# Optimization experiments

Hardware: AMD Instinct MI355X
Metric: run time of the kernel (lower is better)

## Reference

```python
import jax, jax.numpy as jnp
import numpy as np

B, N, T = 32, 256, 256
W, H, EMB = 32, 128, 64          # window_size, tgcn_hidden_dim, gsl_embed_dim
K, ALPHA, NC, E = 3, 1.0, 16, 8192  # gsl_avg_steps, gsl_alpha, num_classes, static edges
GCN_IN = W + H                    # GSL gconv in_channels
THRESH = 1e-8


def setup_inputs():
    ks = jax.random.split(jax.random.key(0), 24)
    rng = np.random.default_rng(0)
    src = rng.integers(0, N, size=E)
    tgt = (src + 1 + rng.integers(0, N - 1, size=E)) % N  # no self-loops (PyG adds them)
    edge_index = jnp.asarray(np.stack([src, tgt]), dtype=jnp.int32)

    def p(k, shape):
        return jax.random.normal(k, shape, jnp.float32) * (shape[0] ** -0.5)

    z = lambda n: jnp.zeros((n,), jnp.float32)
    return {
        "x": jax.random.normal(ks[0], (B, N, T), jnp.float32),
        "static_edge_index": edge_index,
        "static_edge_weight": jax.random.uniform(ks[1], (E,), jnp.float32),
        "Wg": p(ks[2], (GCN_IN, EMB)), "bg": z(EMB),
        "W1": p(ks[3], (EMB, EMB)), "b1": z(EMB),
        "W2": p(ks[4], (EMB, EMB)), "b2": z(EMB),
        "Wz": p(ks[5], (W, H)), "bz": z(H),
        "Wr": p(ks[6], (W, H)), "br": z(H),
        "Wh": p(ks[7], (W, H)), "bh": z(H),
        "Wlz": p(ks[8], (2 * H, H)), "blz": z(H),
        "Wlr": p(ks[9], (2 * H, H)), "blr": z(H),
        "Wlh": p(ks[10], (2 * H, H)), "blh": z(H),
        "Wc": p(ks[11], (H * N, NC)), "bc": z(NC),
    }


def _forward(x, edge_index, edge_weight, Wg, bg, W1, b1, W2, b2,
             Wz, bz, Wr, br, Wh, bh, Wlz, blz, Wlr, blr, Wlh, blh, Wc, bc):
    dt = x.dtype
    eye = jnp.eye(N, dtype=dt)

    # Static graph: dense adjacency + self loops, symmetric GCN normalization.
    A = jnp.zeros((N, N), dt).at[edge_index[0], edge_index[1]].add(edge_weight) + eye
    deg = A.sum(0)  # in-degree at targets (col sums)
    di = jnp.where(deg > 0, jax.lax.rsqrt(deg), 0.0)
    S = di[:, None] * A * di[None, :]  # S[r,c]; out[c] = sum_r S[r,c] x[r]

    # windowing: v[t,b,n,:] = x[b,n,t*W:(t+1)*W]
    v = x.reshape(B, N, T // W, W).transpose(2, 0, 1, 3)  # [nw,B,N,W]

    def gcn_norm_b(Ad):  # Ad [B,N,N], zero diagonal guaranteed
        Ah = Ad + eye
        d = Ah.sum(-2)
        q = jnp.where(d > 0, jax.lax.rsqrt(d), 0.0)
        return q[:, :, None] * Ah * q[:, None, :]

    def step(carry, vt):
        h, hist, cnt = carry  # h [B,N,H], hist [K,B,N,N]
        It = jnp.concatenate([vt, h], -1)                   # [B,N,W+H]
        df = jnp.einsum('rc,brf->bcf', S, It @ Wg) + bg     # static GCNConv
        de1 = jnp.tanh(ALPHA * (df @ W1 + b1))
        de2 = jnp.tanh(ALPHA * (df @ W2 + b2))
        M = jnp.einsum('bne,bme->bnm', de1, de2)            # de1 @ de2^T
        Et = jax.nn.relu(jnp.tanh(ALPHA * (M - M.transpose(0, 2, 1))))
        hist = jnp.concatenate([hist[1:], Et[None]], 0)     # deque(maxlen=K)
        cnt = jnp.minimum(cnt + 1, K)
        Mt = hist.sum(0) / cnt.astype(dt)
        An = gcn_norm_b(jnp.where(Mt > THRESH, Mt, jnp.zeros((), dt)))

        def conv(Wk, bk):  # dynamic GCNConv, block-diag == per-batch dense
            return jnp.einsum('brc,brf->bcf', An, vt @ Wk) + bk

        Z = jax.nn.sigmoid(jnp.concatenate([conv(Wz, bz), h], -1) @ Wlz + blz)
        R = jax.nn.sigmoid(jnp.concatenate([conv(Wr, br), h], -1) @ Wlr + blr)
        Ht = jnp.tanh(jnp.concatenate([conv(Wh, bh), h * R], -1) @ Wlh + blh)
        h = Z * h + (1.0 - Z) * Ht
        return (h, hist, cnt), None

    h0 = jnp.zeros((B, N, H), dt)
    hist0 = jnp.zeros((K, B, N, N), dt)
    (h, _, _), _ = jax.lax.scan(step, (h0, hist0, jnp.int32(0)), v)
    return h.reshape(B, N * H) @ Wc + bc  # [B, NC]


def reference(x, static_edge_index, static_edge_weight, Wg, bg, W1, b1, W2, b2,
              Wz, bz, Wr, br, Wh, bh, Wlz, blz, Wlr, blr, Wlh, blh, Wc, bc):
    return _forward(x, static_edge_index, static_edge_weight, Wg, bg, W1, b1, W2, b2,
                    Wz, bz, Wr, br, Wh, bh, Wlz, blz, Wlr, blr, Wlh, blh, Wc, bc)
```

## Files before the change

### kernel.cpp

```cpp
#include <hip/hip_runtime.h>
#include <hip/hip_bf16.h>
#include <math.h>

#define BB  32
#define NN  256
#define TT  256
#define WW  32
#define HH  128
#define EMBD 64
#define NCLS 16
#define NE  8192

__device__ __forceinline__ float bf(const __hip_bfloat16* p, int i) {
    return __bfloat162float(p[i]);
}
__device__ __forceinline__ float ld3(const void* p, int i, int m) {
    if (m == 2) return (float)((const double*)p)[i];
    if (m == 1) return ((const float*)p)[i];
    return __bfloat162float(((const __hip_bfloat16*)p)[i]);
}
__device__ __forceinline__ float r16(float x) {
    return __bfloat162float(__float2bfloat16(x));
}
__device__ __forceinline__ float tanh_s(float x) {
    x = fminf(20.0f, fmaxf(-20.0f, x));
    return tanhf(x);
}
__device__ __forceinline__ float sig_s(float x) {
    x = fminf(30.0f, fmaxf(-30.0f, x));
    return 1.0f / (1.0f + expf(-x));
}


__global__ __launch_bounds__(64) void k_sentinel(float* out, float v) {
    int i = blockIdx.x * 64 + threadIdx.x;
    if (i < BB * NCLS) out[i] = v;
}

__global__ __launch_bounds__(256) void k_probe_all(
        const void* x, const void* ew, const void* Wg, const void* W1, const void* W2,
        const void* Wz, const void* Wr, const void* Wh, const void* Wlz, const void* Wlr,
        const void* Wlh, const void* Wc, int* insB, int* insF) {
    int sec = blockIdx.x >> 2, sub = blockIdx.x & 3;
    const void* p; int nB, idx;
    switch (sec) {
        case 0:  p = x;   nB = 32768; idx = 0;  break;
        case 1:  p = ew;  nB = 8192;  idx = 2;  break;
        case 2:  p = Wg;  nB = 10240; idx = 3;  break;
        case 3:  p = W1;  nB = 4096;  idx = 5;  break;
        case 4:  p = W2;  nB = 4096;  idx = 7;  break;
        case 5:  p = Wz;  nB = 4096;  idx = 9;  break;
        case 6:  p = Wr;  nB = 4096;  idx = 11; break;
        case 7:  p = Wh;  nB = 4096;  idx = 13; break;
        case 8:  p = Wlz; nB = 32768; idx = 15; break;
        case 9:  p = Wlr; nB = 32768; idx = 17; break;
        case 10: p = Wlh; nB = 32768; idx = 19; break;
        default: p = Wc;  nB = 32768; idx = 21; break;
    }
    int nF = nB >> 2;
    const __hip_bfloat16* pb = (const __hip_bfloat16*)p;
    const float* pf = (const float*)p;
    int start = sub * 256 + threadIdx.x;
    for (int i = start; i < nB; i += 1024) {
        float v = __bfloat162float(pb[i]);
        if (!(fabsf(v) < 64.0f)) { insB[idx] = 1; break; }
    }
    for (int i = start; i < nF; i += 1024) {
        float v = pf[i];
        if (!(fabsf(v) < 1e4f)) { insF[idx] = 1; break; }
    }
}

__global__ void k_resolve(const int* insB, const int* insF, int* modes) {
    int i = threadIdx.x;
    if (i < 32 && i != 1)
        modes[i] = insB[i] ? (insF[i] ? 2 : 1) : 0;
}

__global__ __launch_bounds__(64) void k_detect_ei(const int* ei, int* modes) {
    if (threadIdx.x == 0 && blockIdx.x == 0) {
        bool allz = true;
        for (int k = 1; k < 64; k += 2) if (ei[k] != 0) allz = false;
        modes[1] = allz ? 1 : 0;
    }
}

__global__ __launch_bounds__(256) void k_cvtall(const void* Wg, const void* W1, const void* W2,
                                                const void* Wz, const void* Wr, const void* Wh,
                                                const void* Wlz, const void* Wlr, const void* Wlh,
                                                const void* Wc, const int* modes, float* dst) {
    int i = blockIdx.x * 256 + threadIdx.x;
    if (i >= 665600) return;
    float v;
    if      (i < 10240)  v = ld3(Wg,  i,          modes[3]);
    else if (i < 14336)  v = ld3(W1,  i - 10240,  modes[5]);
    else if (i < 18432)  v = ld3(W2,  i - 14336,  modes[7]);
    else if (i < 22528)  v = ld3(Wz,  i - 18432,  modes[9]);
    else if (i < 26624)  v = ld3(Wr,  i - 22528,  modes[11]);
    else if (i < 30720)  v = ld3(Wh,  i - 26624,  modes[13]);
    else if (i < 63488)  v = ld3(Wlz, i - 30720,  modes[15]);
    else if (i < 96256)  v = ld3(Wlr, i - 63488,  modes[17]);
    else if (i < 129024) v = ld3(Wlh, i - 96256,  modes[19]);
    else if (i < 653312) v = ld3(Wc,  i - 129024, modes[21]);
    else {
        int j = i - 653312, w = j / 384, rem = j - w * 384;
        int g = rem >> 7, f = rem & 127;
        const void* Wk = (g == 0) ? Wz : ((g == 1) ? Wr : Wh);
        int mk = (g == 0) ? modes[9] : ((g == 1) ? modes[11] : modes[13]);
        v = ld3(Wk, w * 128 + f, mk);
    }
    dst[i] = v;
}

__global__ __launch_bounds__(256) void k_fuse(const float* Wzf, const float* Wrf, const float* Whf,
                                              const float* Wlzf, const float* Wlrf, const float* Wlhf,
                                              const __hip_bfloat16* bz, const __hip_bfloat16* br,
                                              const __hip_bfloat16* bh,
                                              const __hip_bfloat16* blz, const __hip_bfloat16* blr,
                                              const __hip_bfloat16* blh,
                                              float* Wf, float* bfv) {
    int g = blockIdx.y;
    const float* Wcv = (g == 0) ? Wzf : ((g == 1) ? Wrf : Whf);
    const float* Wl  = (g == 0) ? Wlzf : ((g == 1) ? Wlrf : Wlhf);
    const __hip_bfloat16* bcv = (g == 0) ? bz : ((g == 1) ? br : bh);
    const __hip_bfloat16* blv = (g == 0) ? blz : ((g == 1) ? blr : blh);
    int idx = blockIdx.x * 256 + threadIdx.x;
    if (idx >= 160 * 128) return;
    int k = idx >> 7, f = idx & 127;
    float v;
    if (k < 32) {
        float acc = 0.f;
        for (int m = 0; m < 128; m++) acc += Wcv[k * 128 + m] * Wl[m * 128 + f];
        v = acc;
    } else {
        v = Wl[(k + 96) * 128 + f];
    }
    Wf[((size_t)g * 160 + k) * 128 + f] = v;
    if (idx < 128) {
        float acc = __bfloat162float(blv[idx]);
        for (int m = 0; m < 128; m++) acc += __bfloat162float(bcv[m]) * Wl[m * 128 + idx];
        bfv[g * 128 + idx] = acc;
    }
}


__global__ __launch_bounds__(256) void k_scatter(const int* ei, const void* ew, float* A,
                                                 const int* modes) {
    int e = blockIdx.x * 256 + threadIdx.x;
    if (e < NE) {
        int s, t;
        if (modes[1]) { s = ei[2 * e]; t = ei[2 * (NE + e)]; }
        else          { s = ei[e];     t = ei[NE + e]; }
        float w = r16(ld3(ew, e, modes[2]));
        if ((unsigned)s < NN && (unsigned)t < NN)
            atomicAdd(&A[s * NN + t], w);
    }
    if (blockIdx.x == 0) atomicAdd(&A[threadIdx.x * NN + threadIdx.x], 1.0f);
}

__global__ __launch_bounds__(256) void k_roundA(float* A) {
    int i = blockIdx.x * 256 + threadIdx.x;
    A[i] = r16(A[i]);
}

__global__ __launch_bounds__(256) void k_di(const float* A, float* di) {
    int wave = threadIdx.x >> 6, lane = threadIdx.x & 63;
    int c = blockIdx.x * 4 + wave;
    float s = 0.f;
    for (int r = lane; r < NN; r += 64) s += A[r * NN + c];
    for (int o = 32; o > 0; o >>= 1) s += __shfl_down(s, o, 64);
    if (lane == 0) {
        float deg = r16(s);
        di[c] = (deg > 0.f) ? r16(1.0f / sqrtf(deg)) : 0.0f;
    }
}

__global__ __launch_bounds__(256) void k_St(const float* A, const float* di, float* St) {
    int idx = blockIdx.x * 256 + threadIdx.x;
    int c = idx >> 8, r = idx & 255;
    St[idx] = r16(r16(di[r] * A[r * NN + c]) * di[c]);
}


__global__ __launch_bounds__(256) void k1_itwg4(const void* x, const float* h,
                                                const float* Wgf, float* Y,
                                                int t, const int* modes) {
    __shared__ float vt[4][32];
    __shared__ float hr[4][128];
    int b = blockIdx.y, n0 = blockIdx.x * 4;
    int tid = threadIdx.x;
    int nd = tid >> 6, f = tid & 63;
    if (f < WW) vt[nd][f] = ld3(x, (b * NN + n0 + nd) * TT + t * WW + f, modes[0]);
    size_t hb = (size_t)(b * NN + n0 + nd) * HH;
    hr[nd][f] = h[hb + f];
    hr[nd][f + 64] = h[hb + f + 64];
    __syncthreads();
    float acc = 0.f;
    for (int k = 0; k < WW; k++)  acc += vt[nd][k] * Wgf[k * EMBD + f];
    for (int k = 0; k < HH; k++)  acc += hr[nd][k] * Wgf[(WW + k) * EMBD + f];
    if (t == 0 && modes[0] == 0 && modes[3] == 0) acc = r16(acc);
    Y[(size_t)(b * NN + n0 + nd) * EMBD + f] = acc;
}

__global__ __launch_bounds__(256) void k23g(const float* St, const float* Y,
                                            const __hip_bfloat16* bg,
                                            const float* W1f, const float* W2f,
                                            const __hip_bfloat16* b1, const __hip_bfloat16* b2,
                                            float* de1, float* de2, float* qsum,
                                            int t, const int* modes) {
    __shared__ float As[32][36];
    __shared__ float Bs[32][68];
    __shared__ float dfT[64][36];
    int b = blockIdx.y, c0 = blockIdx.x * 32;
    int tid = threadIdx.x;
    if (blockIdx.x == 0) qsum[b * NN + tid] = 0.f;
    int tm = tid >> 4, tn = tid & 15;
    int am = tid & 31, ak0 = (tid >> 5) * 4;
    int bk = tid >> 3, bn0 = (tid & 7) * 8;
    const float* Yb = Y + (size_t)b * (NN * EMBD);
    float acc[2][4] = {};
    for (int kb = 0; kb < 256; kb += 32) {
        float4 a0 = *(const float4*)(St + (size_t)(c0 + am) * 256 + kb + ak0);
        float av4[4] = {a0.x, a0.y, a0.z, a0.w};
        int rot = (tid >> 5) & 3;
#pragma unroll
        for (int jj = 0; jj < 4; jj++) { int j = (jj + rot) & 3; As[ak0 + j][am] = av4[j]; }
        const float* bp = Yb + (size_t)(kb + bk) * 64 + bn0;
        *(float4*)&Bs[bk][bn0]     = *(const float4*)bp;
        *(float4*)&Bs[bk][bn0 + 4] = *(const float4*)(bp + 4);
        __syncthreads();
#pragma unroll
        for (int kk = 0; kk < 32; kk++) {
            float2 av = *(const float2*)&As[kk][tm * 2];
            float4 bv = *(const float4*)&Bs[kk][tn * 4];
            float aa[2] = {av.x, av.y};
            float bb[4] = {bv.x, bv.y, bv.z, bv.w};
#pragma unroll
            for (int i = 0; i < 2; i++)
#pragma unroll
                for (int j = 0; j < 4; j++) acc[i][j] += aa[i] * bb[j];
        }
        __syncthreads();
    }
    bool rnd = (t == 0 && modes[0] == 0 && modes[3] == 0);
#pragma unroll
    for (int i = 0; i < 2; i++)
#pragma unroll
        for (int j = 0; j < 4; j++) {
            int f = tn * 4 + j;
            float v = (rnd ? r16(acc[i][j]) : acc[i][j]) + bf(bg, f);
            dfT[f][tm * 2 + i] = v;
        }
    __syncthreads();
    float a1acc[2][4] = {};
    for (int kb2 = 0; kb2 < 64; kb2 += 32) {
        const float* bp = W1f + (size_t)(kb2 + bk) * 64 + bn0;
        *(float4*)&Bs[bk][bn0]     = *(const float4*)bp;
        *(float4*)&Bs[bk][bn0 + 4] = *(const float4*)(bp + 4);
        __syncthreads();
#pragma unroll
        for (int kk = 0; kk < 32; kk++) {
            float2 av = *(const float2*)&dfT[kb2 + kk][tm * 2];
            float4 bv = *(const float4*)&Bs[kk][tn * 4];
            float aa[2] = {av.x, av.y};
            float bb[4] = {bv.x, bv.y, bv.z, bv.w};
#pragma unroll
            for (int i = 0; i < 2; i++)
#pragma unroll
                for (int j = 0; j < 4; j++) a1acc[i][j] += aa[i] * bb[j];
        }
        __syncthreads();
    }
#pragma unroll
    for (int i = 0; i < 2; i++) {
        int row = b * NN + c0 + tm * 2 + i;
        float4 o;
        o.x = tanh_s(a1acc[i][0] + bf(b1, tn * 4 + 0));
        o.y = tanh_s(a1acc[i][1] + bf(b1, tn * 4 + 1));
        o.z = tanh_s(a1acc[i][2] + bf(b1, tn * 4 + 2));
        o.w = tanh_s(a1acc[i][3] + bf(b1, tn * 4 + 3));
        *(float4*)&de1[(size_t)row * 64 + tn * 4] = o;
    }
    float a2acc[2][4] = {};
    for (int kb2 = 0; kb2 < 64; kb2 += 32) {
        const float* bp = W2f + (size_t)(kb2 + bk) * 64 + bn0;
        *(float4*)&Bs[bk][bn0]     = *(const float4*)bp;
        *(float4*)&Bs[bk][bn0 + 4] = *(const float4*)(bp + 4);
        __syncthreads();
#pragma unroll
        for (int kk = 0; kk < 32; kk++) {
            float2 av = *(const float2*)&dfT[kb2 + kk][tm * 2];
            float4 bv = *(const float4*)&Bs[kk][tn * 4];
            float aa[2] = {av.x, av.y};
            float bb[4] = {bv.x, bv.y, bv.z, bv.w};
#pragma unroll
            for (int i = 0; i < 2; i++)
#pragma unroll
                for (int j = 0; j < 4; j++) a2acc[i][j] += aa[i] * bb[j];
        }
        __syncthreads();
    }
#pragma unroll
    for (int i = 0; i < 2; i++) {
        int row = b * NN + c0 + tm * 2 + i;
        float4 o;
        o.x = tanh_s(a2acc[i][0] + bf(b2, tn * 4 + 0));
        o.y = tanh_s(a2acc[i][1] + bf(b2, tn * 4 + 1));
        o.z = tanh_s(a2acc[i][2] + bf(b2, tn * 4 + 2));
        o.w = tanh_s(a2acc[i][3] + bf(b2, tn * 4 + 3));
        *(float4*)&de2[(size_t)row * 64 + tn * 4] = o;
    }
}

__global__ __launch_bounds__(256) void k45(const float* de1, const float* de2,
                                           float* hist, float* AhT, float* qsum,
                                           int slabW, int slabR, float inv_cnt) {
    __shared__ float As[32][68];
    __shared__ float Bs[32][68];
    __shared__ float m2b[64][65];
    __shared__ float qpart[64];
    int b = blockIdx.z, r0 = blockIdx.x * 64, c0 = blockIdx.y * 64;
    int tid = threadIdx.x;
    if (tid < 64) qpart[tid] = 0.f;
    int tn = tid & 15, tm = tid >> 4;
    int am = tid >> 2, ak0 = (tid & 3) * 8;
    int rot = (tid & 3) * 2;
    const float* d1 = de1 + (size_t)b * (NN * EMBD);
    const float* d2 = de2 + (size_t)b * (NN * EMBD);
    float acc2[4][4] = {};
    for (int kb = 0; kb < 64; kb += 32) {
        const float* ap = d1 + (size_t)(c0 + am) * 64 + kb + ak0;
        float4 a0 = *(const float4*)ap;
        float4 a1 = *(const float4*)(ap + 4);
        float av8[8] = {a0.x, a0.y, a0.z, a0.w, a1.x, a1.y, a1.z, a1.w};
#pragma unroll
        for (int jj = 0; jj < 8; jj++) { int j = (jj + rot) & 7; As[ak0 + j][am] = av8[j]; }
        const float* bp = d2 + (size_t)(r0 + am) * 64 + kb + ak0;
        float4 b0 = *(const float4*)bp;
        float4 b1v = *(const float4*)(bp + 4);
        float bv8[8] = {b0.x, b0.y, b0.z, b0.w, b1v.x, b1v.y, b1v.z, b1v.w};
#pragma unroll
        for (int jj = 0; jj < 8; jj++) { int j = (jj + rot) & 7; Bs[ak0 + j][am] = bv8[j]; }
        __syncthreads();
#pragma unroll
        for (int kk = 0; kk < 32; kk++) {
            float4 av = *(const float4*)&As[kk][tm * 4];
            float4 bv = *(const float4*)&Bs[kk][tn * 4];
            float aa[4] = {av.x, av.y, av.z, av.w};
            float bb[4] = {bv.x, bv.y, bv.z, bv.w};
#pragma unroll
            for (int i = 0; i < 4; i++)
#pragma unroll
                for (int j = 0; j < 4; j++) acc2[i][j] += aa[i] * bb[j];
        }
        __syncthreads();
    }
#pragma unroll
    for (int i = 0; i < 4; i++)
#pragma unroll
        for (int j = 0; j < 4; j++) m2b[tm * 4 + i][tn * 4 + j] = acc2[i][j];
    float acc1[4][4] = {};
    for (int kb = 0; kb < 64; kb += 32) {
        const float* ap = d1 + (size_t)(r0 + am) * 64 + kb + ak0;
        float4 a0 = *(const float4*)ap;
        float4 a1 = *(const float4*)(ap + 4);
        float av8[8] = {a0.x, a0.y, a0.z, a0.w, a1.x, a1.y, a1.z, a1.w};
#pragma unroll
        for (int jj = 0; jj < 8; jj++) { int j = (jj + rot) & 7; As[ak0 + j][am] = av8[j]; }
        const float* bp = d2 + (size_t)(c0 + am) * 64 + kb + ak0;
        float4 b0 = *(const float4*)bp;
        float4 b1v = *(const float4*)(bp + 4);
        float bv8[8] = {b0.x, b0.y, b0.z, b0.w, b1v.x, b1v.y, b1v.z, b1v.w};
#pragma unroll
        for (int jj = 0; jj < 8; jj++) { int j = (jj + rot) & 7; Bs[ak0 + j][am] = bv8[j]; }
        __syncthreads();
#pragma unroll
        for (int kk = 0; kk < 32; kk++) {
            float4 av = *(const float4*)&As[kk][tm * 4];
            float4 bv = *(const float4*)&Bs[kk][tn * 4];
            float aa[4] = {av.x, av.y, av.z, av.w};
            float bb[4] = {bv.x, bv.y, bv.z, bv.w};
#pragma unroll
            for (int i = 0; i < 4; i++)
#pragma unroll
                for (int j = 0; j < 4; j++) acc1[i][j] += aa[i] * bb[j];
        }
        __syncthreads();
    }
    size_t NB = (size_t)BB * NN * NN;
    float* hsW = hist + (size_t)slabW * NB;
    const float* hsR = hist + (size_t)slabR * NB;
    float ad[4][4];
#pragma unroll
    for (int i = 0; i < 4; i++) {
        int r = r0 + tm * 4 + i;
        size_t o = ((size_t)(b * NN + r)) * NN + c0 + tn * 4;
        float4 e2v = *(const float4*)&hsW[o];
        float4 e1v = *(const float4*)&hsR[o];
        float e2a[4] = {e2v.x, e2v.y, e2v.z, e2v.w};
        float e1a[4] = {e1v.x, e1v.y, e1v.z, e1v.w};
        float4 ew4;
        float eo[4];
#pragma unroll
        for (int j = 0; j < 4; j++) {
            int c = c0 + tn * 4 + j;
            float e = tanh_s(acc1[i][j] - m2b[tn * 4 + j][tm * 4 + i]);
            e = e > 0.f ? e : 0.f;
            eo[j] = e;
            float mt = (e + e1a[j] + e2a[j]) * inv_cnt;
            float adv = (mt > 1e-8f) ? mt : 0.f;
            if (r == c) adv += 1.f;
            ad[i][j] = adv;
        }
        ew4.x = eo[0]; ew4.y = eo[1]; ew4.z = eo[2]; ew4.w = eo[3];
        *(float4*)&hsW[o] = ew4;
    }
#pragma unroll
    for (int j = 0; j < 4; j++) {
        float cs = ad[0][j] + ad[1][j] + ad[2][j] + ad[3][j];
        atomicAdd(&qpart[tn * 4 + j], cs);
    }
    __syncthreads();
#pragma unroll
    for (int i = 0; i < 4; i++)
#pragma unroll
        for (int j = 0; j < 4; j++) m2b[tn * 4 + j][tm * 4 + i] = ad[i][j];
    __syncthreads();
#pragma unroll
    for (int kk = 0; kk < 4; kk++) {
        int e = tid + kk * 256;
        int cl = e >> 4, q4 = e & 15;
        float4 o;
        o.x = m2b[cl][q4 * 4 + 0]; o.y = m2b[cl][q4 * 4 + 1];
        o.z = m2b[cl][q4 * 4 + 2]; o.w = m2b[cl][q4 * 4 + 3];
        *(float4*)&AhT[((size_t)(b * NN + c0 + cl)) * NN + r0 + q4 * 4] = o;
    }
    if (tid < 64) atomicAdd(&qsum[b * NN + c0 + tid], qpart[tid]);
}

__global__ __launch_bounds__(256) void k8a(const float* AhT, const void* x, const float* qsum,
                                           float* G, int t, const int* modes) {
    __shared__ float As[32][36];
    __shared__ float Bs[32][36];
    int b = blockIdx.y, c0 = blockIdx.x * 32;
    int tid = threadIdx.x;
    int tm = tid >> 3, tn = tid & 7;
    int am = tid & 31, ak0 = (tid >> 5) * 8;
    int rB = tid >> 3, w0 = (tid & 7) * 4;
    int m0 = modes[0];
    const float* Ab = AhT + (size_t)b * (NN * NN);
    float acc[4] = {0, 0, 0, 0};
    for (int kb = 0; kb < 256; kb += 32) {
        const float* ap = Ab + (size_t)(c0 + am) * 256 + kb + ak0;
        float4 a0 = *(const float4*)ap;
        float4 a1 = *(const float4*)(ap + 4);
        float av8[8] = {a0.x, a0.y, a0.z, a0.w, a1.x, a1.y, a1.z, a1.w};
#pragma unroll
        for (int j = 0; j < 8; j++) As[ak0 + j][am] = av8[j];
        int r = kb + rB;
        float qr = 1.0f / sqrtf(fmaxf(qsum[b * NN + r], 1e-12f));
        int xbase = (b * NN + r) * TT + t * WW + w0;
        float pv[4];
#pragma unroll
        for (int i = 0; i < 4; i++) pv[i] = qr * ld3(x, xbase + i, m0);
        int rot = rB & 3;
#pragma unroll
        for (int i = 0; i < 4; i++) {
            int j = (i + rot) & 3;
            Bs[rB][w0 + j] = pv[j];
        }
        __syncthreads();
#pragma unroll
        for (int kk = 0; kk < 32; kk++) {
            float a = As[kk][tm];
            float4 bv = *(const float4*)&Bs[kk][tn * 4];
            acc[0] += a * bv.x; acc[1] += a * bv.y;
            acc[2] += a * bv.z; acc[3] += a * bv.w;
        }
        __syncthreads();
    }
    int c = c0 + tm;
    float qc = 1.0f / sqrtf(fmaxf(qsum[b * NN + c], 1e-12f));
    float4 o = make_float4(qc * acc[0], qc * acc[1], qc * acc[2], qc * acc[3]);
    *(float4*)&G[((size_t)(b * NN + c)) * 32 + tn * 4] = o;
}

__global__ __launch_bounds__(256) void kZR(const float* G, const float* h,
                                           const float* Wf, const float* bfv,
                                           float* Z, float* hR) {
    __shared__ float As[160 * 33];
    __shared__ float Bs[32 * 128];
    int r0 = blockIdx.x * 32;
    int g  = blockIdx.y;
    int tid = threadIdx.x;
    {
        int r = tid >> 3, c4 = (tid & 7) * 4;
        float4 gv = *(const float4*)&G[(size_t)(r0 + r) * 32 + c4];
        As[(c4 + 0) * 33 + r] = gv.x;
        As[(c4 + 1) * 33 + r] = gv.y;
        As[(c4 + 2) * 33 + r] = gv.z;
        As[(c4 + 3) * 33 + r] = gv.w;
    }
#pragma unroll
    for (int u = 0; u < 4; u++) {
        int e = tid + u * 256;
        int r = e >> 5, c4 = (e & 31) * 4;
        float4 hv = *(const float4*)&h[(size_t)(r0 + r) * 128 + c4];
        As[(32 + c4 + 0) * 33 + r] = hv.x;
        As[(32 + c4 + 1) * 33 + r] = hv.y;
        As[(32 + c4 + 2) * 33 + r] = hv.z;
        As[(32 + c4 + 3) * 33 + r] = hv.w;
    }
    const float* Wgp = Wf + (size_t)g * (160 * 128);
    int rg = tid >> 5, cg = tid & 31;
    float acc[4][4] = {};
    for (int kb = 0; kb < 160; kb += 32) {
#pragma unroll
        for (int u = 0; u < 4; u++) {
            int e = tid + u * 256;
            int kk = e >> 5, c4 = (e & 31) * 4;
            *(float4*)&Bs[kk * 128 + c4] = *(const float4*)&Wgp[(size_t)(kb + kk) * 128 + c4];
        }
        __syncthreads();
#pragma unroll 4
        for (int kk = 0; kk < 32; kk++) {
            const float* ap = &As[(kb + kk) * 33 + rg * 4];
            float a0 = ap[0], a1 = ap[1], a2 = ap[2], a3 = ap[3];
            float4 bv = *(const float4*)&Bs[kk * 128 + cg * 4];
            acc[0][0] += a0 * bv.x; acc[0][1] += a0 * bv.y; acc[0][2] += a0 * bv.z; acc[0][3] += a0 * bv.w;
            acc[1][0] += a1 * bv.x; acc[1][1] += a1 * bv.y; acc[1][2] += a1 * bv.z; acc[1][3] += a1 * bv.w;
            acc[2][0] += a2 * bv.x; acc[2][1] += a2 * bv.y; acc[2][2] += a2 * bv.z; acc[2][3] += a2 * bv.w;
            acc[3][0] += a3 * bv.x; acc[3][1] += a3 * bv.y; acc[3][2] += a3 * bv.z; acc[3][3] += a3 * bv.w;
        }
        __syncthreads();
    }
    float bb[4];
#pragma unroll
    for (int j = 0; j < 4; j++) bb[j] = bfv[g * 128 + cg * 4 + j];
#pragma unroll
    for (int i = 0; i < 4; i++) {
        int row = r0 + rg * 4 + i;
        float4 o;
        o.x = sig_s(acc[i][0] + bb[0]);
        o.y = sig_s(acc[i][1] + bb[1]);
        o.z = sig_s(acc[i][2] + bb[2]);
        o.w = sig_s(acc[i][3] + bb[3]);
        if (g == 0) {
            *(float4*)&Z[(size_t)row * 128 + cg * 4] = o;
        } else {
            float4 hv = *(const float4*)&h[(size_t)row * 128 + cg * 4];
            o.x *= hv.x; o.y *= hv.y; o.z *= hv.z; o.w *= hv.w;
            *(float4*)&hR[(size_t)row * 128 + cg * 4] = o;
        }
    }
}

__global__ __launch_bounds__(256) void kHt(const float* G, float* h, const float* hR,
                                           const float* Z, const float* Wf, const float* bfv) {
    __shared__ float As[160 * 33];
    __shared__ float Bs[32 * 128];
    int r0 = blockIdx.x * 32;
    int tid = threadIdx.x;
    {
        int r = tid >> 3, c4 = (tid & 7) * 4;
        float4 gv = *(const float4*)&G[(size_t)(r0 + r) * 32 + c4];
        As[(c4 + 0) * 33 + r] = gv.x;
        As[(c4 + 1) * 33 + r] = gv.y;
        As[(c4 + 2) * 33 + r] = gv.z;
        As[(c4 + 3) * 33 + r] = gv.w;
    }
#pragma unroll
    for (int u = 0; u < 4; u++) {
        int e = tid + u * 256;
        int r = e >> 5, c4 = (e & 31) * 4;
        float4 hv = *(const float4*)&hR[(size_t)(r0 + r) * 128 + c4];
        As[(32 + c4 + 0) * 33 + r] = hv.x;
        As[(32 + c4 + 1) * 33 + r] = hv.y;
        As[(32 + c4 + 2) * 33 + r] = hv.z;
        As[(32 + c4 + 3) * 33 + r] = hv.w;
    }
    const float* Wgp = Wf + (size_t)2 * (160 * 128);
    int rg = tid >> 5, cg = tid & 31;
    float acc[4][4] = {};
    for (int kb = 0; kb < 160; kb += 32) {
#pragma unroll
        for (int u = 0; u < 4; u++) {
            int e = tid + u * 256;
            int kk = e >> 5, c4 = (e & 31) * 4;
            *(float4*)&Bs[kk * 128 + c4] = *(const float4*)&Wgp[(size_t)(kb + kk) * 128 + c4];
        }
        __syncthreads();
#pragma unroll 4
        for (int kk = 0; kk < 32; kk++) {
            const float* ap = &As[(kb + kk) * 33 + rg * 4];
            float a0 = ap[0], a1 = ap[1], a2 = ap[2], a3 = ap[3];
            float4 bv = *(const float4*)&Bs[kk * 128 + cg * 4];
            acc[0][0] += a0 * bv.x; acc[0][1] += a0 * bv.y; acc[0][2] += a0 * bv.z; acc[0][3] += a0 * bv.w;
            acc[1][0] += a1 * bv.x; acc[1][1] += a1 * bv.y; acc[1][2] += a1 * bv.z; acc[1][3] += a1 * bv.w;
            acc[2][0] += a2 * bv.x; acc[2][1] += a2 * bv.y; acc[2][2] += a2 * bv.z; acc[2][3] += a2 * bv.w;
            acc[3][0] += a3 * bv.x; acc[3][1] += a3 * bv.y; acc[3][2] += a3 * bv.z; acc[3][3] += a3 * bv.w;
        }
        __syncthreads();
    }
    float bb[4];
#pragma unroll
    for (int j = 0; j < 4; j++) bb[j] = bfv[256 + cg * 4 + j];
#pragma unroll
    for (int i = 0; i < 4; i++) {
        int row = r0 + rg * 4 + i;
        size_t o = (size_t)row * 128 + cg * 4;
        float4 zv = *(const float4*)&Z[o];
        float4 hv = *(const float4*)&h[o];
        float4 r;
        r.x = zv.x * hv.x + (1.0f - zv.x) * tanh_s(acc[i][0] + bb[0]);
        r.y = zv.y * hv.y + (1.0f - zv.y) * tanh_s(acc[i][1] + bb[1]);
        r.z = zv.z * hv.z + (1.0f - zv.z) * tanh_s(acc[i][2] + bb[2]);
        r.w = zv.w * hv.w + (1.0f - zv.w) * tanh_s(acc[i][3] + bb[3]);
        *(float4*)&h[o] = r;
    }
}

__global__ __launch_bounds__(256) void k10a(const float* h, const float* Wcf, float* partial) {
    __shared__ float red[16][17];
    int chunk = blockIdx.x, b = blockIdx.y;
    int c = threadIdx.x & 15, isub = threadIdx.x >> 4;
    const float* hb = h + (size_t)b * (NN * HH);
    int i0 = chunk * 2048;
    float acc = 0.f;
    for (int s = 0; s < 128; s++) {
        int i = i0 + isub + 16 * s;
        acc += hb[i] * Wcf[(size_t)i * NCLS + c];
    }
    red[isub][c] = acc;
    __syncthreads();
    for (int st = 8; st > 0; st >>= 1) {
        if (isub < st) red[isub][c] += red[isub + st][c];
        __syncthreads();
    }
    if (isub == 0) partial[((size_t)(b * NCLS + c)) * 16 + chunk] = red[0][c];
}

__global__ __launch_bounds__(512) void k10b(const float* partial, const __hip_bfloat16* bcb,
                                            float* out) {
    int tid = threadIdx.x;
    if (tid < BB * NCLS) {
        int c = tid & 15;
        float s = 0.f;
        for (int k = 0; k < 16; k++) s += partial[(size_t)tid * 16 + k];
        out[tid] = s + bf(bcb, c);
    }
}


extern "C" void kernel_launch(void* const* d_in, const int* in_sizes, int n_in,
                              void* d_out, int out_size, void* d_ws, size_t ws_size,
                              hipStream_t stream) {
    float* out = (float*)d_out;

    static const int exp_sizes[23] = {2097152, 16384, 8192, 10240, 64, 4096, 64, 4096, 64,
                                      4096, 128, 4096, 128, 4096, 128, 32768, 128, 32768, 128,
                                      32768, 128, 524288, 16};
    if (n_in != 23) { k_sentinel<<<8, 64, 0, stream>>>(out, 4444.0f); return; }
    for (int i = 0; i < 23; i++) {
        if (in_sizes[i] != exp_sizes[i]) {
            k_sentinel<<<8, 64, 0, stream>>>(out, (float)(4000 + i));
            return;
        }
    }

    const void* x   = d_in[0];
    const int*  ei  = (const int*)d_in[1];
    const void* ew  = d_in[2];
    const void* Wg  = d_in[3];
    const __hip_bfloat16* bg  = (const __hip_bfloat16*)d_in[4];
    const void* W1  = d_in[5];
    const __hip_bfloat16* b1  = (const __hip_bfloat16*)d_in[6];
    const void* W2  = d_in[7];
    const __hip_bfloat16* b2  = (const __hip_bfloat16*)d_in[8];
    const void* Wz  = d_in[9];
    const __hip_bfloat16* bz  = (const __hip_bfloat16*)d_in[10];
    const void* Wr  = d_in[11];
    const __hip_bfloat16* br  = (const __hip_bfloat16*)d_in[12];
    const void* Wh  = d_in[13];
    const __hip_bfloat16* bh  = (const __hip_bfloat16*)d_in[14];
    const void* Wlz = d_in[15];
    const __hip_bfloat16* blz = (const __hip_bfloat16*)d_in[16];
    const void* Wlr = d_in[17];
    const __hip_bfloat16* blr = (const __hip_bfloat16*)d_in[18];
    const void* Wlh = d_in[19];
    const __hip_bfloat16* blh = (const __hip_bfloat16*)d_in[20];
    const void* Wc  = d_in[21];
    const __hip_bfloat16* bcb = (const __hip_bfloat16*)d_in[22];

    float* ws = (float*)d_ws;
    const size_t off_A    = 0;
    const size_t off_hist = off_A + 65536;
    const size_t off_h    = off_hist + 2u * 2097152;
    const size_t off_flag = off_h + 1048576;
    const size_t off_mode = off_flag + 16;
    const size_t off_insB = off_mode + 32;
    const size_t off_insF = off_insB + 32;
    const size_t zero_end = off_insF + 32;
    const size_t off_St   = zero_end;
    const size_t off_di   = off_St + 65536;
    const size_t off_q    = off_di + 256;
    const size_t off_AhT  = off_q + 8192;
    const size_t off_Yp   = off_AhT + 2097152;
    const size_t off_C    = off_Yp + 3145728;
    const size_t off_wts  = off_C + 3145728;
    const size_t off_hR   = off_wts + 665600;
    const size_t need_bytes = (off_hR + 1048576u) * sizeof(float);

    if (ws_size < need_bytes) {
        k_sentinel<<<8, 64, 0, stream>>>(out, (float)ws_size);
        return;
    }

    float* A    = ws + off_A;
    float* hist = ws + off_hist;
    float* h    = ws + off_h;
    int*   modes= (int*)(ws + off_mode);
    int*   insB = (int*)(ws + off_insB);
    int*   insF = (int*)(ws + off_insF);
    float* St   = ws + off_St;
    float* di   = ws + off_di;
    float* qsum = ws + off_q;
    float* AhT  = ws + off_AhT;
    float* wts  = ws + off_wts;
    float* Y    = ws + off_Yp;
    float* de1  = ws + off_Yp + 1048576;
    float* de2  = ws + off_Yp + 1572864;
    float* Z    = ws + off_Yp + 1048576;
    float* G    = ws + off_Yp + 2097152;
    float* hR   = ws + off_hR;
    float* Wf   = ws + off_C;
    float* bfv  = ws + off_C + 61440;
    float* partial = qsum;

    float* Wgf  = wts;
    float* W1f  = wts + 10240;
    float* W2f  = wts + 14336;
    float* Wzf  = wts + 18432;
    float* Wrf  = wts + 22528;
    float* Whf  = wts + 26624;
    float* Wlzf = wts + 30720;
    float* Wlrf = wts + 63488;
    float* Wlhf = wts + 96256;
    float* Wcf  = wts + 129024;

    hipMemsetAsync(ws, 0, zero_end * sizeof(float), stream);

    k_probe_all<<<48, 256, 0, stream>>>(x, ew, Wg, W1, W2, Wz, Wr, Wh, Wlz, Wlr, Wlh, Wc,
                                        insB, insF);
    k_resolve<<<1, 32, 0, stream>>>(insB, insF, modes);
    k_detect_ei<<<1, 64, 0, stream>>>(ei, modes);
    k_cvtall<<<2600, 256, 0, stream>>>(Wg, W1, W2, Wz, Wr, Wh, Wlz, Wlr, Wlh, Wc, modes, wts);
    k_fuse<<<dim3(80, 3), 256, 0, stream>>>(Wzf, Wrf, Whf, Wlzf, Wlrf, Wlhf,
                                            bz, br, bh, blz, blr, blh, Wf, bfv);

    k_scatter<<<NE / 256, 256, 0, stream>>>(ei, ew, A, modes);
    k_roundA<<<NN * NN / 256, 256, 0, stream>>>(A);
    k_di<<<NN / 4, 256, 0, stream>>>(A, di);
    k_St<<<NN * NN / 256, 256, 0, stream>>>(A, di, St);

    for (int t = 0; t < 8; t++) {
        k1_itwg4<<<dim3(NN / 4, BB), 256, 0, stream>>>(x, h, Wgf, Y, t, modes);
        k23g<<<dim3(8, BB), 256, 0, stream>>>(St, Y, bg, W1f, W2f, b1, b2,
                                              de1, de2, qsum, t, modes);
        float inv_cnt = 1.0f / (float)((t + 1 < 3) ? (t + 1) : 3);
        k45<<<dim3(4, 4, BB), 256, 0, stream>>>(de1, de2, hist, AhT, qsum,
                                                t & 1, (t + 1) & 1, inv_cnt);
        k8a<<<dim3(NN / 32, BB), 256, 0, stream>>>(AhT, x, qsum, G, t, modes);
        kZR<<<dim3(NN * BB / 32, 2), 256, 0, stream>>>(G, h, Wf, bfv, Z, hR);
        kHt<<<NN * BB / 32, 256, 0, stream>>>(G, h, hR, Z, Wf, bfv);
    }

    k10a<<<dim3(16, BB), 256, 0, stream>>>(h, Wcf, partial);
    k10b<<<1, 512, 0, stream>>>(partial, bcb, out);
}
```

Measured before the change: 948.9 us.

## Fuse GRU gates, update, and next-step Wg projection into one kernel

Merges the Z/R gate kernel and the candidate/update kernel into a single per-row-tile kernel. Z and R stay in registers, and h*R is formed in shared memory instead of going through global Z and hR buffers. The same kernel then loads the next window of x and computes the next step's Y = [x_{t+1}, h] @ Wg, so the separate k1 launch is dropped for t>0. This cuts global round trips and launches per step. In exchange the grid is halved (no gate-parallel y dimension), and each block runs three serial GEMMs plus the Y projection, which lowers parallelism.

```diff
diff --git a/kernel.cpp b/kernel.cpp
--- a/kernel.cpp
+++ b/kernel.cpp
@@ -485,14 +485,16 @@
     *(float4*)&G[((size_t)(b * NN + c)) * 32 + tn * 4] = o;
 }
 
-__global__ __launch_bounds__(256) void kZR(const float* G, const float* h,
-                                           const float* Wf, const float* bfv,
-                                           float* Z, float* hR) {
+__global__ __launch_bounds__(256) void kZRH(const float* G, float* h,
+                                            const float* Wf, const float* bfv,
+                                            const float* Wgf, const void* x, float* Y,
+                                            int t, const int* modes) {
     __shared__ float As[160 * 33];
     __shared__ float Bs[32 * 128];
     int r0 = blockIdx.x * 32;
-    int g  = blockIdx.y;
+    int b  = r0 >> 8;
     int tid = threadIdx.x;
+    int m0 = modes[0];
     {
         int r = tid >> 3, c4 = (tid & 7) * 4;
         float4 gv = *(const float4*)&G[(size_t)(r0 + r) * 32 + c4];
@@ -511,113 +513,122 @@
         As[(32 + c4 + 2) * 33 + r] = hv.z;
         As[(32 + c4 + 3) * 33 + r] = hv.w;
     }
-    const float* Wgp = Wf + (size_t)g * (160 * 128);
     int rg = tid >> 5, cg = tid & 31;
+    float zv[4][4], rv[4][4];
+    for (int g = 0; g < 2; g++) {
+        const float* Wgp = Wf + (size_t)g * (160 * 128);
+        float acc[4][4] = {};
+        for (int kb = 0; kb < 160; kb += 32) {
+#pragma unroll
+            for (int u = 0; u < 4; u++) {
+                int e = tid + u * 256;
+                int kk = e >> 5, c4 = (e & 31) * 4;
+                *(float4*)&Bs[kk * 128 + c4] = *(const float4*)&Wgp[(size_t)(kb + kk) * 128 + c4];
+            }
+            __syncthreads();
+#pragma unroll 4
+            for (int kk = 0; kk < 32; kk++) {
+                const float* ap = &As[(kb + kk) * 33 + rg * 4];
+                float a0 = ap[0], a1 = ap[1], a2 = ap[2], a3 = ap[3];
+                float4 bv = *(const float4*)&Bs[kk * 128 + cg * 4];
+                acc[0][0] += a0 * bv.x; acc[0][1] += a0 * bv.y; acc[0][2] += a0 * bv.z; acc[0][3] += a0 * bv.w;
+                acc[1][0] += a1 * bv.x; acc[1][1] += a1 * bv.y; acc[1][2] += a1 * bv.z; acc[1][3] += a1 * bv.w;
+                acc[2][0] += a2 * bv.x; acc[2][1] += a2 * bv.y; acc[2][2] += a2 * bv.z; acc[2][3] += a2 * bv.w;
+                acc[3][0] += a3 * bv.x; acc[3][1] += a3 * bv.y; acc[3][2] += a3 * bv.z; acc[3][3] += a3 * bv.w;
+            }
+            __syncthreads();
+        }
+#pragma unroll
+        for (int i = 0; i < 4; i++)
+#pragma unroll
+            for (int j = 0; j < 4; j++) {
+                float v = sig_s(acc[i][j] + bfv[g * 128 + cg * 4 + j]);
+                if (g == 0) zv[i][j] = v; else rv[i][j] = v;
+            }
+    }
+#pragma unroll
+    for (int i = 0; i < 4; i++)
+#pragma unroll
+        for (int j = 0; j < 4; j++) {
+            int slot = (32 + cg * 4 + j) * 33 + rg * 4 + i;
+            As[slot] = As[slot] * rv[i][j];
+        }
+    __syncthreads();
     float acc[4][4] = {};
-    for (int kb = 0; kb < 160; kb += 32) {
-#pragma unroll
-        for (int u = 0; u < 4; u++) {
-            int e = tid + u * 256;
-            int kk = e >> 5, c4 = (e & 31) * 4;
-            *(float4*)&Bs[kk * 128 + c4] = *(const float4*)&Wgp[(size_t)(kb + kk) * 128 + c4];
-        }
-        __syncthreads();
+    {
+        const float* Wgp = Wf + (size_t)2 * (160 * 128);
+        for (int kb = 0; kb < 160; kb += 32) {
+#pragma unroll
+            for (int u = 0; u < 4; u++) {
+                int e = tid + u * 256;
+                int kk = e >> 5, c4 = (e & 31) * 4;
+                *(float4*)&Bs[kk * 128 + c4] = *(const float4*)&Wgp[(size_t)(kb + kk) * 128 + c4];
+            }
+            __syncthreads();
 #pragma unroll 4
-        for (int kk = 0; kk < 32; kk++) {
-            const float* ap = &As[(kb + kk) * 33 + rg * 4];
-            float a0 = ap[0], a1 = ap[1], a2 = ap[2], a3 = ap[3];
-            float4 bv = *(const float4*)&Bs[kk * 128 + cg * 4];
-            acc[0][0] += a0 * bv.x; acc[0][1] += a0 * bv.y; acc[0][2] += a0 * bv.z; acc[0][3] += a0 * bv.w;
-            acc[1][0] += a1 * bv.x; acc[1][1] += a1 * bv.y; acc[1][2] += a1 * bv.z; acc[1][3] += a1 * bv.w;
-            acc[2][0] += a2 * bv.x; acc[2][1] += a2 * bv.y; acc[2][2] += a2 * bv.z; acc[2][3] += a2 * bv.w;
-            acc[3][0] += a3 * bv.x; acc[3][1] += a3 * bv.y; acc[3][2] += a3 * bv.z; acc[3][3] += a3 * bv.w;
-        }
-        __syncthreads();
-    }
-    float bb[4];
-#pragma unroll
-    for (int j = 0; j < 4; j++) bb[j] = bfv[g * 128 + cg * 4 + j];
-#pragma unroll
-    for (int i = 0; i < 4; i++) {
-        int row = r0 + rg * 4 + i;
-        float4 o;
-        o.x = sig_s(acc[i][0] + bb[0]);
-        o.y = sig_s(acc[i][1] + bb[1]);
-        o.z = sig_s(acc[i][2] + bb[2]);
-        o.w = sig_s(acc[i][3] + bb[3]);
-        if (g == 0) {
-            *(float4*)&Z[(size_t)row * 128 + cg * 4] = o;
-        } else {
-            float4 hv = *(const float4*)&h[(size_t)row * 128 + cg * 4];
-            o.x *= hv.x; o.y *= hv.y; o.z *= hv.z; o.w *= hv.w;
-            *(float4*)&hR[(size_t)row * 128 + cg * 4] = o;
-        }
-    }
-}
-
-__global__ __launch_bounds__(256) void kHt(const float* G, float* h, const float* hR,
-                                           const float* Z, const float* Wf, const float* bfv) {
-    __shared__ float As[160 * 33];
-    __shared__ float Bs[32 * 128];
-    int r0 = blockIdx.x * 32;
-    int tid = threadIdx.x;
-    {
-        int r = tid >> 3, c4 = (tid & 7) * 4;
-        float4 gv = *(const float4*)&G[(size_t)(r0 + r) * 32 + c4];
-        As[(c4 + 0) * 33 + r] = gv.x;
-        As[(c4 + 1) * 33 + r] = gv.y;
-        As[(c4 + 2) * 33 + r] = gv.z;
-        As[(c4 + 3) * 33 + r] = gv.w;
-    }
-#pragma unroll
-    for (int u = 0; u < 4; u++) {
-        int e = tid + u * 256;
-        int r = e >> 5, c4 = (e & 31) * 4;
-        float4 hv = *(const float4*)&hR[(size_t)(r0 + r) * 128 + c4];
-        As[(32 + c4 + 0) * 33 + r] = hv.x;
-        As[(32 + c4 + 1) * 33 + r] = hv.y;
-        As[(32 + c4 + 2) * 33 + r] = hv.z;
-        As[(32 + c4 + 3) * 33 + r] = hv.w;
-    }
-    const float* Wgp = Wf + (size_t)2 * (160 * 128);
-    int rg = tid >> 5, cg = tid & 31;
-    float acc[4][4] = {};
-    for (int kb = 0; kb < 160; kb += 32) {
-#pragma unroll
-        for (int u = 0; u < 4; u++) {
-            int e = tid + u * 256;
-            int kk = e >> 5, c4 = (e & 31) * 4;
-            *(float4*)&Bs[kk * 128 + c4] = *(const float4*)&Wgp[(size_t)(kb + kk) * 128 + c4];
-        }
-        __syncthreads();
-#pragma unroll 4
-        for (int kk = 0; kk < 32; kk++) {
-            const float* ap = &As[(kb + kk) * 33 + rg * 4];
-            float a0 = ap[0], a1 = ap[1], a2 = ap[2], a3 = ap[3];
-            float4 bv = *(const float4*)&Bs[kk * 128 + cg * 4];
-            acc[0][0] += a0 * bv.x; acc[0][1] += a0 * bv.y; acc[0][2] += a0 * bv.z; acc[0][3] += a0 * bv.w;
-            acc[1][0] += a1 * bv.x; acc[1][1] += a1 * bv.y; acc[1][2] += a1 * bv.z; acc[1][3] += a1 * bv.w;
-            acc[2][0] += a2 * bv.x; acc[2][1] += a2 * bv.y; acc[2][2] += a2 * bv.z; acc[2][3] += a2 * bv.w;
-            acc[3][0] += a3 * bv.x; acc[3][1] += a3 * bv.y; acc[3][2] += a3 * bv.z; acc[3][3] += a3 * bv.w;
-        }
-        __syncthreads();
-    }
-    float bb[4];
-#pragma unroll
-    for (int j = 0; j < 4; j++) bb[j] = bfv[256 + cg * 4 + j];
+            for (int kk = 0; kk < 32; kk++) {
+                const float* ap = &As[(kb + kk) * 33 + rg * 4];
+                float a0 = ap[0], a1 = ap[1], a2 = ap[2], a3 = ap[3];
+                float4 bv = *(const float4*)&Bs[kk * 128 + cg * 4];
+                acc[0][0] += a0 * bv.x; acc[0][1] += a0 * bv.y; acc[0][2] += a0 * bv.z; acc[0][3] += a0 * bv.w;
+                acc[1][0] += a1 * bv.x; acc[1][1] += a1 * bv.y; acc[1][2] += a1 * bv.z; acc[1][3] += a1 * bv.w;
+                acc[2][0] += a2 * bv.x; acc[2][1] += a2 * bv.y; acc[2][2] += a2 * bv.z; acc[2][3] += a2 * bv.w;
+                acc[3][0] += a3 * bv.x; acc[3][1] += a3 * bv.y; acc[3][2] += a3 * bv.z; acc[3][3] += a3 * bv.w;
+            }
+            __syncthreads();
+        }
+    }
 #pragma unroll
     for (int i = 0; i < 4; i++) {
         int row = r0 + rg * 4 + i;
         size_t o = (size_t)row * 128 + cg * 4;
-        float4 zv = *(const float4*)&Z[o];
         float4 hv = *(const float4*)&h[o];
         float4 r;
-        r.x = zv.x * hv.x + (1.0f - zv.x) * tanh_s(acc[i][0] + bb[0]);
-        r.y = zv.y * hv.y + (1.0f - zv.y) * tanh_s(acc[i][1] + bb[1]);
-        r.z = zv.z * hv.z + (1.0f - zv.z) * tanh_s(acc[i][2] + bb[2]);
-        r.w = zv.w * hv.w + (1.0f - zv.w) * tanh_s(acc[i][3] + bb[3]);
+        r.x = zv[i][0] * hv.x + (1.0f - zv[i][0]) * tanh_s(acc[i][0] + bfv[256 + cg * 4 + 0]);
+        r.y = zv[i][1] * hv.y + (1.0f - zv[i][1]) * tanh_s(acc[i][1] + bfv[256 + cg * 4 + 1]);
+        r.z = zv[i][2] * hv.z + (1.0f - zv[i][2]) * tanh_s(acc[i][2] + bfv[256 + cg * 4 + 2]);
+        r.w = zv[i][3] * hv.w + (1.0f - zv[i][3]) * tanh_s(acc[i][3] + bfv[256 + cg * 4 + 3]);
         *(float4*)&h[o] = r;
-    }
+        As[(32 + cg * 4 + 0) * 33 + rg * 4 + i] = r.x;
+        As[(32 + cg * 4 + 1) * 33 + rg * 4 + i] = r.y;
+        As[(32 + cg * 4 + 2) * 33 + rg * 4 + i] = r.z;
+        As[(32 + cg * 4 + 3) * 33 + rg * 4 + i] = r.w;
+    }
+    if (t < 7) {
+#pragma unroll
+        for (int u = 0; u < 4; u++) {
+            int e = tid + u * 256;
+            int r = e >> 5, w = e & 31;
+            As[w * 33 + r] = ld3(x, (r0 + r) * TT + (t + 1) * WW + w, m0);
+        }
+        __syncthreads();
+        int yr = tid >> 3, yc8 = (tid & 7) * 8;
+        float yacc[8] = {};
+        for (int kb = 0; kb < 160; kb += 32) {
+#pragma unroll
+            for (int u = 0; u < 2; u++) {
+                int e = tid + u * 256;
+                int kk = e >> 3, c8 = (e & 7) * 8;
+                const float* wp = Wgf + (size_t)(kb + kk) * 64 + c8;
+                *(float4*)&Bs[kk * 64 + c8]     = *(const float4*)wp;
+                *(float4*)&Bs[kk * 64 + c8 + 4] = *(const float4*)(wp + 4);
+            }
+            __syncthreads();
+#pragma unroll 4
+            for (int kk = 0; kk < 32; kk++) {
+                float a = As[(kb + kk) * 33 + yr];
+                float4 b0 = *(const float4*)&Bs[kk * 64 + yc8];
+                float4 b1 = *(const float4*)&Bs[kk * 64 + yc8 + 4];
+                yacc[0] += a * b0.x; yacc[1] += a * b0.y; yacc[2] += a * b0.z; yacc[3] += a * b0.w;
+                yacc[4] += a * b1.x; yacc[5] += a * b1.y; yacc[6] += a * b1.z; yacc[7] += a * b1.w;
+            }
+            __syncthreads();
+        }
+        float* yp = &Y[(size_t)(r0 + yr) * 64 + yc8];
+        *(float4*)yp       = make_float4(yacc[0], yacc[1], yacc[2], yacc[3]);
+        *(float4*)(yp + 4) = make_float4(yacc[4], yacc[5], yacc[6], yacc[7]);
+    }
+    (void)b;
 }
 
 __global__ __launch_bounds__(256) void k10a(const float* h, const float* Wcf, float* partial) {
@@ -730,9 +741,7 @@
     float* Y    = ws + off_Yp;
     float* de1  = ws + off_Yp + 1048576;
     float* de2  = ws + off_Yp + 1572864;
-    float* Z    = ws + off_Yp + 1048576;
     float* G    = ws + off_Yp + 2097152;
-    float* hR   = ws + off_hR;
     float* Wf   = ws + off_C;
     float* bfv  = ws + off_C + 61440;
     float* partial = qsum;
@@ -764,15 +773,15 @@
     k_St<<<NN * NN / 256, 256, 0, stream>>>(A, di, St);
 
     for (int t = 0; t < 8; t++) {
-        k1_itwg4<<<dim3(NN / 4, BB), 256, 0, stream>>>(x, h, Wgf, Y, t, modes);
+        if (t == 0)
+            k1_itwg4<<<dim3(NN / 4, BB), 256, 0, stream>>>(x, h, Wgf, Y, 0, modes);
         k23g<<<dim3(8, BB), 256, 0, stream>>>(St, Y, bg, W1f, W2f, b1, b2,
                                               de1, de2, qsum, t, modes);
         float inv_cnt = 1.0f / (float)((t + 1 < 3) ? (t + 1) : 3);
         k45<<<dim3(4, 4, BB), 256, 0, stream>>>(de1, de2, hist, AhT, qsum,
                                                 t & 1, (t + 1) & 1, inv_cnt);
         k8a<<<dim3(NN / 32, BB), 256, 0, stream>>>(AhT, x, qsum, G, t, modes);
-        kZR<<<dim3(NN * BB / 32, 2), 256, 0, stream>>>(G, h, Wf, bfv, Z, hR);
-        kHt<<<NN * BB / 32, 256, 0, stream>>>(G, h, hR, Z, Wf, bfv);
+        kZRH<<<NN * BB / 32, 256, 0, stream>>>(G, h, Wf, bfv, Wgf, x, Y, t, modes);
     }
 
     k10a<<<dim3(16, BB), 256, 0, stream>>>(h, Wcf, partial);
```

New measurement: 960.5 us. About the same (+1.2%).
